# Performance work log

Hardware: AMD Instinct MI355X
Metric: run time of the kernel (lower is better)

The kernel has to match this reference:

```python
import jax, jax.numpy as jnp
import numpy as np

HEADS = 16
DIM_HEAD = 64
SCALE = DIM_HEAD ** -0.5


def setup_inputs() -> dict:
    key = jax.random.key(0)
    ks = jax.random.split(key, 7)
    B, Nq, Dq = 16, 4096, 1024
    Nc, Dc = 77, 768
    inner = HEADS * DIM_HEAD  # 1024
    return {
        "x": jax.random.normal(ks[0], (B, Nq, Dq), jnp.float32),
        "context": jax.random.normal(ks[1], (B, Nc, Dc), jnp.float32),
        "Wq": jax.random.normal(ks[2], (Dq, inner), jnp.float32) * (Dq ** -0.5),
        "Wk": jax.random.normal(ks[3], (Dc, inner), jnp.float32) * (Dc ** -0.5),
        "Wv": jax.random.normal(ks[4], (Dc, inner), jnp.float32) * (Dc ** -0.5),
        "Wo": jax.random.normal(ks[5], (inner, Dq), jnp.float32) * (inner ** -0.5),
        "bo": jnp.zeros((Dq,), jnp.float32),
    }


def reference(x, context, Wq, Wk, Wv, Wo, bo):
    B, Nq, _ = x.shape
    Nc = context.shape[1]
    # projections (no bias), split heads: [B, H, N, Dh]
    q = (x @ Wq).reshape(B, Nq, HEADS, DIM_HEAD).transpose(0, 2, 1, 3)
    k = (context @ Wk).reshape(B, Nc, HEADS, DIM_HEAD).transpose(0, 2, 1, 3)
    v = (context @ Wv).reshape(B, Nc, HEADS, DIM_HEAD).transpose(0, 2, 1, 3)
    sim = jnp.einsum('bhid,bhjd->bhij', q, k) * SCALE
    attn = jax.nn.softmax(sim, axis=-1)
    out = jnp.einsum('bhij,bhjd->bhid', attn, v)
    out = out.transpose(0, 2, 1, 3).reshape(B, Nq, HEADS * DIM_HEAD)
    # to_out linear (dropout is identity at eval)
    return out @ Wo + bo
```

## Files before the change

### kernel.cpp

```cpp
#include <hip/hip_runtime.h>

typedef unsigned short u16;
typedef __bf16 bf16x8 __attribute__((ext_vector_type(8)));
typedef unsigned short u16x8 __attribute__((ext_vector_type(8)));
typedef float f32x4 __attribute__((ext_vector_type(4)));

namespace {
constexpr int kB = 16;
constexpr int kHeads = 16, kDh = 64;
constexpr int kNcPadS = 80;
constexpr int kNcPadV = 96;

constexpr size_t oWqT = 0;
constexpr size_t oWoT = oWqT + (size_t)1024 * 1024 * 2;
constexpr size_t oWkT = oWoT + (size_t)1024 * 1024 * 2;
constexpr size_t oWvT = oWkT + (size_t)1024 * 768 * 2;
constexpr size_t oCtx = oWvT + (size_t)1024 * 768 * 2;
constexpr size_t oKp  = oCtx + (size_t)1232 * 768 * 2;
constexpr size_t oVp  = oKp + (size_t)kB * kHeads * kNcPadS * kDh * 2;
constexpr size_t oQ   = oVp + (size_t)kB * kHeads * kDh * kNcPadV * 2;
}

__device__ __forceinline__ u16 f2b(float f) {
    __bf16 h = (__bf16)f;
    return __builtin_bit_cast(u16, h);
}
__device__ __forceinline__ bf16x8 ldfrag(const u16* p) {
    return __builtin_bit_cast(bf16x8, *reinterpret_cast<const u16x8*>(p));
}
__device__ __forceinline__ f32x4 mfma16(bf16x8 a, bf16x8 b, f32x4 c) {
    return __builtin_amdgcn_mfma_f32_16x16x32_bf16(a, b, c, 0, 0, 0);
}
__device__ __forceinline__ void gload16(const u16* g, u16* lds) {
    __builtin_amdgcn_global_load_lds(
        (const __attribute__((address_space(1))) void*)g,
        (__attribute__((address_space(3))) void*)lds, 16, 0, 0);
}

#define VMCNT(N) asm volatile("s_waitcnt vmcnt(" #N ")" ::: "memory")
#define BARRIER  do { __builtin_amdgcn_s_barrier(); asm volatile("" ::: "memory"); } while (0)

__device__ __forceinline__ void stage_u(const u16* gp, u16* unit, int tid, int kt) {
#pragma unroll
    for (int i = 0; i < 2; ++i) {
        int g = tid + i * 512;
        int prs = g >> 3;
        int s0 = (g & 7) ^ (prs & 7);
        gload16(gp + (size_t)(prs * 2 + (s0 >> 2)) * 1024 + kt + (s0 & 3) * 8,
                unit + ((g >> 6) << 9));
    }
}
__device__ __forceinline__ int pp16(int row16, int k32) {
    return (row16 >> 1) * 64 + (((((row16 & 1) << 2) | (k32 >> 3)) ^ ((row16 >> 1) & 7)) * 8) + (k32 & 7);
}

__global__ __launch_bounds__(256) void xconv_kernel(const float* __restrict__ x, u16* __restrict__ xb) {
    size_t i = (size_t)blockIdx.x * 256 + threadIdx.x;
    const float4* s = reinterpret_cast<const float4*>(x) + 2 * i;
    float4 v0 = s[0], v1 = s[1];
    u16x8 pk = { f2b(v0.x), f2b(v0.y), f2b(v0.z), f2b(v0.w),
                 f2b(v1.x), f2b(v1.y), f2b(v1.z), f2b(v1.w) };
    *reinterpret_cast<u16x8*>(xb + 8 * i) = pk;
}

__global__ __launch_bounds__(256) void prep2_kernel(
    const float* __restrict__ Wq, const float* __restrict__ Wk,
    const float* __restrict__ Wv, const float* __restrict__ Wo,
    const float* __restrict__ ctx, u16* __restrict__ ws) {
    __shared__ u16 tl[64][72];
    int b = blockIdx.x;
    int tid = threadIdx.x;
    if (b < 896) {
        const float* S; u16* D; int t, DC;
        if (b < 256)       { S = Wq; D = ws + oWqT / 2; t = b;       DC = 1024; }
        else if (b < 512)  { S = Wo; D = ws + oWoT / 2; t = b - 256; DC = 1024; }
        else if (b < 704)  { S = Wk; D = ws + oWkT / 2; t = b - 512; DC = 768;  }
        else               { S = Wv; D = ws + oWvT / 2; t = b - 704; DC = 768;  }
        int tk = t >> 4, tn = t & 15;
        int k0 = tk * 64, n0 = tn * 64;
#pragma unroll
        for (int i = 0; i < 4; ++i) {
            int r = (tid >> 4) + i * 16;
            float4 v = *reinterpret_cast<const float4*>(S + (size_t)(k0 + r) * 1024 + n0 + (tid & 15) * 4);
            u16 e0 = f2b(v.x), e1 = f2b(v.y), e2 = f2b(v.z), e3 = f2b(v.w);
            u16* p = &tl[r][(tid & 15) * 4];
            p[0] = e0; p[1] = e1; p[2] = e2; p[3] = e3;
        }
        __syncthreads();
#pragma unroll
        for (int i = 0; i < 2; ++i) {
            int n = (tid >> 3) + i * 32;
            u16x8 o;
#pragma unroll
            for (int j = 0; j < 8; ++j) o[j] = tl[(tid & 7) * 8 + j][n];
            *reinterpret_cast<u16x8*>(D + (size_t)(n0 + n) * DC + k0 + (tid & 7) * 8) = o;
        }
        return;
    }
    if (b < 896 + 462) {
        size_t i = (size_t)(b - 896) * 2048 + tid * 8;
        const float4* s = reinterpret_cast<const float4*>(ctx) + i / 4;
        float4 v0 = s[0], v1 = s[1];
        u16x8 pk = { f2b(v0.x), f2b(v0.y), f2b(v0.z), f2b(v0.w),
                     f2b(v1.x), f2b(v1.y), f2b(v1.z), f2b(v1.w) };
        *reinterpret_cast<u16x8*>(ws + oCtx / 2 + i) = pk;
        return;
    }
    size_t j = (size_t)(b - 896 - 462) * 2048 + tid * 8;
    u16x8 z = {0, 0, 0, 0, 0, 0, 0, 0};
    *reinterpret_cast<u16x8*>(ws + oKp / 2 + j) = z;
}

__global__ __launch_bounds__(64) void kv_kernel(u16* __restrict__ ws) {
    const u16* ctxb = ws + oCtx / 2;
    const u16* WkT = ws + oWkT / 2;
    const u16* WvT = ws + oWvT / 2;
    u16* Kp = ws + oKp / 2;
    u16* Vp = ws + oVp / 2;
    int l = threadIdx.x;
    int mt = blockIdx.x >> 6;
    int nt = blockIdx.x & 63;
    int rowA = mt * 16 + (l & 15);
    int rowB = nt * 16 + (l & 15);
    int koff = (l >> 4) * 8;
    f32x4 accK = {0.f, 0.f, 0.f, 0.f}, accV = {0.f, 0.f, 0.f, 0.f};
    for (int k = 0; k < 768; k += 32) {
        bf16x8 a  = ldfrag(ctxb + rowA * 768 + k + koff);
        bf16x8 bk = ldfrag(WkT + rowB * 768 + k + koff);
        bf16x8 bv = ldfrag(WvT + rowB * 768 + k + koff);
        accK = mfma16(a, bk, accK);
        accV = mfma16(a, bv, accV);
    }
    int c = nt * 16 + (l & 15);
    int h = c >> 6, d = c & 63;
#pragma unroll
    for (int r = 0; r < 4; ++r) {
        int row = mt * 16 + (l >> 4) * 4 + r;
        int b = row / 77, j = row - b * 77;
        Kp[((size_t)(b * 16 + h) * kNcPadS + j) * kDh + d] = f2b(accK[r] * 0.125f);
        Vp[((size_t)(b * 16 + h) * kDh + d) * kNcPadV + j] = f2b(accV[r]);
    }
}

#define GPHASE(RLO, KS, READB, STAGE, VM) do {                                  \
    if (READB) { _Pragma("unroll") for (int c = 0; c < 4; ++c)                  \
        fb[c] = ldfrag(bU##KS + (wn * 4 + c) * 512 + rdoff); }                  \
    _Pragma("unroll") for (int r = 0; r < 4; ++r)                               \
        fa[r] = ldfrag(aU##KS + (wm * 8 + (RLO) + r) * 512 + rdoff);            \
    STAGE;                                                                      \
    BARRIER;                                                                    \
    __builtin_amdgcn_s_setprio(1);                                              \
    _Pragma("unroll") for (int r = 0; r < 4; ++r)                               \
        _Pragma("unroll") for (int c = 0; c < 4; ++c)                           \
            acc[(RLO) + r][c] = mfma16(fa[r], fb[c], acc[(RLO) + r][c]);        \
    __builtin_amdgcn_s_setprio(0);                                              \
    VM;                                                                         \
    BARRIER;                                                                    \
} while (0)

#define GEMM_LOOP(aGp, bGp)                                                                          \
    stage_u(aGp, &sm[0][0][0][0], tid, 0);                                                           \
    stage_u(bGp, &sm[1][0][0][0], tid, 0);                                                           \
    stage_u(aGp, &sm[0][0][1][0], tid, 32);                                                          \
    stage_u(bGp, &sm[1][0][1][0], tid, 32);                                                          \
    stage_u(aGp, &sm[0][1][0][0], tid, 64);                                                          \
    stage_u(bGp, &sm[1][1][0][0], tid, 64);                                                          \
    VMCNT(8); BARRIER;                                                                               \
    for (int t = 0; t < 16; ++t) {                                                                   \
        const int d = t & 1, e = d ^ 1;                                                              \
        const u16* aU0 = &sm[0][d][0][0];                                                            \
        const u16* aU1 = &sm[0][d][1][0];                                                            \
        const u16* bU0 = &sm[1][d][0][0];                                                            \
        const u16* bU1 = &sm[1][d][1][0];                                                            \
        bf16x8 fa[4], fb[4];                                                                         \
        GPHASE(0, 0, true,  { if (t < 15) stage_u(aGp, &sm[0][e][1][0], tid, (t + 1) * 64 + 32); },  \
               {});                                                                                  \
        GPHASE(4, 0, false, { if (t < 15) stage_u(bGp, &sm[1][e][1][0], tid, (t + 1) * 64 + 32); },  \
               { if (t < 15) { VMCNT(8); } else { VMCNT(0); } });                                    \
        GPHASE(0, 1, true,  { if (t < 14) stage_u(aGp, &sm[0][d][0][0], tid, (t + 2) * 64); },       \
               {});                                                                                  \
        GPHASE(4, 1, false, { if (t < 14) stage_u(bGp, &sm[1][d][0][0], tid, (t + 2) * 64); },       \
               { if (t < 14) { VMCNT(8); } else if (t == 14) { VMCNT(4); } });                       \
    }

__global__ __launch_bounds__(512) void qproj_attn_kernel(const u16* __restrict__ xb, u16* __restrict__ ws) {
    __shared__ u16 sm[2][2][2][8192];
    __shared__ u16 Pb[8][1536];
    const u16* WqT = ws + oWqT / 2;
    u16* qb = ws + oQ / 2;
    int tid = threadIdx.x;
    int lane = tid & 63;
    int w = tid >> 6, wm = w >> 2, wn = w & 3;
    int lr = lane & 15, lr2 = lr >> 1;
    const int rdoff = lr2 * 64 + (((((lane & 1) << 2) | (lane >> 4))) ^ lr2) * 8;
    int bid = blockIdx.x;
    int wg = (bid & 7) * 128 + (bid >> 3);
    int bm = wg >> 2, bn = wg & 3;

    const u16* aG = xb + (size_t)(bm * 256) * 1024;
    const u16* bG = WqT + (size_t)(bn * 256) * 1024;

    f32x4 acc[8][4] = {};
    GEMM_LOOP(aG, bG);

    u16* smf = &sm[0][0][0][0];
    u16* qw = smf + (size_t)w * 8192;
    u16* Pw = &Pb[w][0];
    int g = lane >> 4, g8 = g * 8;

#pragma unroll
    for (int r = 0; r < 8; ++r)
#pragma unroll
        for (int c = 0; c < 4; ++c) {
            int d = c * 16 + lr;
            int unit = r * 2 + (d >> 5);
            int k32 = d & 31;
#pragma unroll
            for (int reg = 0; reg < 4; ++reg)
                qw[unit * 512 + pp16(g * 4 + reg, k32)] = f2b(acc[r][c][reg]);
        }
    {
        u16x8 z = {0, 0, 0, 0, 0, 0, 0, 0};
        *reinterpret_cast<u16x8*>(Pw + 2 * 512 + lane * 8) = z;
    }
    int b = bm >> 4;
    int h = bn * 4 + wn;
    const u16* Kh = ws + oKp / 2 + (size_t)(b * 16 + h) * kNcPadS * kDh;
    const u16* Vh = ws + oVp / 2 + (size_t)(b * 16 + h) * kDh * kNcPadV;
    bf16x8 kf[5][2], vf[3][4];
#pragma unroll
    for (int nt = 0; nt < 5; ++nt)
#pragma unroll
        for (int kc = 0; kc < 2; ++kc)
            kf[nt][kc] = ldfrag(Kh + (nt * 16 + lr) * 64 + kc * 32 + g8);
#pragma unroll
    for (int kti = 0; kti < 3; ++kti)
#pragma unroll
        for (int nt = 0; nt < 4; ++nt)
            vf[kti][nt] = ldfrag(Vh + (nt * 16 + lr) * kNcPadV + kti * 32 + g8);
    u16x8 bmask[3];
#pragma unroll
    for (int kti = 0; kti < 3; ++kti)
#pragma unroll
        for (int j = 0; j < 8; ++j)
            bmask[kti][j] = (kti * 32 + g8 + j < 77) ? (u16)0x3F80 : (u16)0;

#pragma unroll 1
    for (int rb = 0; rb < 8; ++rb) {
        f32x4 s[5] = {};
#pragma unroll
        for (int kc = 0; kc < 2; ++kc) {
            bf16x8 a = ldfrag(qw + (rb * 2 + kc) * 512 + rdoff);
#pragma unroll
            for (int nt = 0; nt < 5; ++nt) s[nt] = mfma16(a, kf[nt][kc], s[nt]);
        }
#pragma unroll
        for (int nt = 0; nt < 5; ++nt)
#pragma unroll
            for (int reg = 0; reg < 4; ++reg) {
                int j = nt * 16 + lr;
                Pw[(j >> 5) * 512 + pp16(g * 4 + reg, j & 31)] = f2b(__expf(s[nt][reg]));
            }
        f32x4 o[4] = {};
        f32x4 msum = {0.f, 0.f, 0.f, 0.f};
#pragma unroll
        for (int kti = 0; kti < 3; ++kti) {
            bf16x8 a = ldfrag(Pw + kti * 512 + rdoff);
#pragma unroll
            for (int nt = 0; nt < 4; ++nt) o[nt] = mfma16(a, vf[kti][nt], o[nt]);
            msum = mfma16(a, __builtin_bit_cast(bf16x8, bmask[kti]), msum);
        }
#pragma unroll
        for (int reg = 0; reg < 4; ++reg) {
            float rinv = 1.f / msum[reg];
            int row = bm * 256 + wm * 128 + rb * 16 + g * 4 + reg;
#pragma unroll
            for (int nt = 0; nt < 4; ++nt)
                qb[(size_t)row * 1024 + h * 64 + nt * 16 + lr] = f2b(o[nt][reg] * rinv);
        }
    }
}

__global__ __launch_bounds__(512) void outproj_kernel(u16* __restrict__ ws, const float* __restrict__ bo,
                                                      float* __restrict__ out) {
    __shared__ u16 sm[2][2][2][8192];
    const u16* qb = ws + oQ / 2;
    const u16* WoT = ws + oWoT / 2;
    int tid = threadIdx.x;
    int lane = tid & 63;
    int w = tid >> 6, wm = w >> 2, wn = w & 3;
    int lr = lane & 15, lr2 = lr >> 1;
    const int rdoff = lr2 * 64 + (((((lane & 1) << 2) | (lane >> 4))) ^ lr2) * 8;
    int bid = blockIdx.x;
    int wg = (bid & 7) * 128 + (bid >> 3);
    int bm = wg >> 2, bn = wg & 3;

    const u16* aG = qb + (size_t)(bm * 256) * 1024;
    const u16* bG = WoT + (size_t)(bn * 256) * 1024;

    f32x4 acc[8][4] = {};
    GEMM_LOOP(aG, bG);

#pragma unroll
    for (int c = 0; c < 4; ++c) {
        int col = bn * 256 + wn * 64 + c * 16 + lr;
        float bias = bo[col];
#pragma unroll
        for (int r = 0; r < 8; ++r)
#pragma unroll
            for (int reg = 0; reg < 4; ++reg) {
                int row = bm * 256 + wm * 128 + r * 16 + (lane >> 4) * 4 + reg;
                out[(size_t)row * 1024 + col] = acc[r][c][reg] + bias;
            }
    }
}

extern "C" void kernel_launch(void* const* d_in, const int* in_sizes, int n_in,
                              void* d_out, int out_size, void* d_ws, size_t ws_size,
                              hipStream_t stream) {
    const float* x   = (const float*)d_in[0];
    const float* ctx = (const float*)d_in[1];
    const float* Wq  = (const float*)d_in[2];
    const float* Wk  = (const float*)d_in[3];
    const float* Wv  = (const float*)d_in[4];
    const float* Wo  = (const float*)d_in[5];
    const float* bo  = (const float*)d_in[6];
    float* out = (float*)d_out;
    u16* ws = (u16*)d_ws;
    u16* xb = (u16*)d_out;
    (void)in_sizes; (void)n_in; (void)out_size; (void)ws_size;

    xconv_kernel<<<32768, 256, 0, stream>>>(x, xb);
    prep2_kernel<<<896 + 462 + 1408, 256, 0, stream>>>(Wq, Wk, Wv, Wo, ctx, ws);
    kv_kernel<<<77 * 64, 64, 0, stream>>>(ws);
    qproj_attn_kernel<<<1024, 512, 0, stream>>>(xb, ws);
    outproj_kernel<<<1024, 512, 0, stream>>>(ws, bo, out);
}
```

Before: 502.9 us.

## Fuse fp32-to-bf16 conversion of x into the Q-projection GEMM loader

Drops the separate xconv kernel. The Q-projection GEMM now loads fp32 x straight into registers, packs it to bf16 and writes it into LDS, using a register-staged prefetch two tiles ahead. The goal is to avoid writing and re-reading a 128MB bf16 copy of x plus one kernel launch. In exchange the A operand is read as fp32, doubling its bytes per GEMM, since each x tile is re-read by 4 column blocks. The pipeline also gains extra register pressure and manual waitcnt bookkeeping.

```diff
diff --git a/kernel.cpp b/kernel.cpp
--- a/kernel.cpp
+++ b/kernel.cpp
@@ -36,8 +36,14 @@
         (const __attribute__((address_space(1))) void*)g,
         (__attribute__((address_space(3))) void*)lds, 16, 0, 0);
 }
+__device__ __forceinline__ u16x8 pk8(float4 a, float4 b) {
+    u16x8 p = { f2b(a.x), f2b(a.y), f2b(a.z), f2b(a.w),
+                f2b(b.x), f2b(b.y), f2b(b.z), f2b(b.w) };
+    return p;
+}
 
 #define VMCNT(N) asm volatile("s_waitcnt vmcnt(" #N ")" ::: "memory")
+#define LGKM0    asm volatile("s_waitcnt lgkmcnt(0)" ::: "memory")
 #define BARRIER  do { __builtin_amdgcn_s_barrier(); asm volatile("" ::: "memory"); } while (0)
 
 __device__ __forceinline__ void stage_u(const u16* gp, u16* unit, int tid, int kt) {
@@ -52,15 +58,6 @@
 }
 __device__ __forceinline__ int pp16(int row16, int k32) {
     return (row16 >> 1) * 64 + (((((row16 & 1) << 2) | (k32 >> 3)) ^ ((row16 >> 1) & 7)) * 8) + (k32 & 7);
-}
-
-__global__ __launch_bounds__(256) void xconv_kernel(const float* __restrict__ x, u16* __restrict__ xb) {
-    size_t i = (size_t)blockIdx.x * 256 + threadIdx.x;
-    const float4* s = reinterpret_cast<const float4*>(x) + 2 * i;
-    float4 v0 = s[0], v1 = s[1];
-    u16x8 pk = { f2b(v0.x), f2b(v0.y), f2b(v0.z), f2b(v0.w),
-                 f2b(v1.x), f2b(v1.y), f2b(v1.z), f2b(v1.w) };
-    *reinterpret_cast<u16x8*>(xb + 8 * i) = pk;
 }
 
 __global__ __launch_bounds__(256) void prep2_kernel(
@@ -101,9 +98,7 @@
         size_t i = (size_t)(b - 896) * 2048 + tid * 8;
         const float4* s = reinterpret_cast<const float4*>(ctx) + i / 4;
         float4 v0 = s[0], v1 = s[1];
-        u16x8 pk = { f2b(v0.x), f2b(v0.y), f2b(v0.z), f2b(v0.w),
-                     f2b(v1.x), f2b(v1.y), f2b(v1.z), f2b(v1.w) };
-        *reinterpret_cast<u16x8*>(ws + oCtx / 2 + i) = pk;
+        *reinterpret_cast<u16x8*>(ws + oCtx / 2 + i) = pk8(v0, v1);
         return;
     }
     size_t j = (size_t)(b - 896 - 462) * 2048 + tid * 8;
@@ -183,7 +178,45 @@
                { if (t < 14) { VMCNT(8); } else if (t == 14) { VMCNT(4); } });                       \
     }
 
-__global__ __launch_bounds__(512) void qproj_attn_kernel(const u16* __restrict__ xb, u16* __restrict__ ws) {
+#define QISS(SET, KT) do {                                                                \
+    SET##0 = *reinterpret_cast<const float4*>(aF0 + (KT));                                \
+    SET##1 = *reinterpret_cast<const float4*>(aF0 + (KT) + 4);                            \
+    SET##2 = *reinterpret_cast<const float4*>(aF1 + (KT));                                \
+    SET##3 = *reinterpret_cast<const float4*>(aF1 + (KT) + 4);                            \
+    SET##4 = *reinterpret_cast<const float4*>(aF0 + (KT) + 32);                           \
+    SET##5 = *reinterpret_cast<const float4*>(aF0 + (KT) + 36);                           \
+    SET##6 = *reinterpret_cast<const float4*>(aF1 + (KT) + 32);                           \
+    SET##7 = *reinterpret_cast<const float4*>(aF1 + (KT) + 36);                           \
+} while (0)
+#define QWRT0(SET, BUF) do {                                                              \
+    u16* u_ = &sm[0][BUF][0][0];                                                          \
+    *reinterpret_cast<u16x8*>(u_ + tid * 8) = pk8(SET##0, SET##1);                        \
+    *reinterpret_cast<u16x8*>(u_ + (tid + 512) * 8) = pk8(SET##2, SET##3);                \
+} while (0)
+#define QWRT1(SET, BUF) do {                                                              \
+    u16* u_ = &sm[0][BUF][1][0];                                                          \
+    *reinterpret_cast<u16x8*>(u_ + tid * 8) = pk8(SET##4, SET##5);                        \
+    *reinterpret_cast<u16x8*>(u_ + (tid + 512) * 8) = pk8(SET##6, SET##7);                \
+} while (0)
+
+#define QTILE(T, CUR, NXT) do {                                                           \
+    const int t_ = (T);                                                                   \
+    const int d = t_ & 1, e = d ^ 1;                                                      \
+    const u16* aU0 = &sm[0][d][0][0];                                                     \
+    const u16* aU1 = &sm[0][d][1][0];                                                     \
+    const u16* bU0 = &sm[1][d][0][0];                                                     \
+    const u16* bU1 = &sm[1][d][1][0];                                                     \
+    bf16x8 fa[4], fb[4];                                                                  \
+    GPHASE(0, 0, true,  { if (t_ + 2 <= 15) QISS(NXT, (t_ + 2) * 64); }, {});             \
+    GPHASE(4, 0, false, { if (t_ + 1 <= 15) stage_u(bG, &sm[1][e][1][0], tid, (t_ + 1) * 64 + 32); }, \
+           { if (t_ <= 13) { VMCNT(12); } else if (t_ == 14) { VMCNT(4); } else { VMCNT(0); } });     \
+    GPHASE(0, 1, true,  {}, { if (t_ + 1 <= 15) { QWRT0(CUR, e); LGKM0; } });             \
+    GPHASE(4, 1, false, { if (t_ + 2 <= 15) stage_u(bG, &sm[1][d][0][0], tid, (t_ + 2) * 64); },      \
+           { if (t_ + 1 <= 15) { QWRT1(CUR, e); LGKM0; }                                  \
+             if (t_ <= 13) { VMCNT(12); } else if (t_ == 14) { VMCNT(2); } });            \
+} while (0)
+
+__global__ __launch_bounds__(512) void qproj_attn_kernel(const float* __restrict__ x, u16* __restrict__ ws) {
     __shared__ u16 sm[2][2][2][8192];
     __shared__ u16 Pb[8][1536];
     const u16* WqT = ws + oWqT / 2;
@@ -197,11 +230,31 @@
     int wg = (bid & 7) * 128 + (bid >> 3);
     int bm = wg >> 2, bn = wg & 3;
 
-    const u16* aG = xb + (size_t)(bm * 256) * 1024;
+    int prs = tid >> 3;
+    int s0 = (tid & 7) ^ (prs & 7);
+    const float* aF0 = x + (size_t)(bm * 256 + prs * 2 + (s0 >> 2)) * 1024 + (s0 & 3) * 8;
+    const float* aF1 = aF0 + (size_t)128 * 1024;
     const u16* bG = WqT + (size_t)(bn * 256) * 1024;
 
     f32x4 acc[8][4] = {};
-    GEMM_LOOP(aG, bG);
+    float4 Aq0, Aq1, Aq2, Aq3, Aq4, Aq5, Aq6, Aq7;
+    float4 Bq0, Bq1, Bq2, Bq3, Bq4, Bq5, Bq6, Bq7;
+
+    QISS(Bq, 0);
+    stage_u(bG, &sm[1][0][0][0], tid, 0);
+    stage_u(bG, &sm[1][0][1][0], tid, 32);
+    QISS(Aq, 64);
+    stage_u(bG, &sm[1][1][0][0], tid, 64);
+    VMCNT(14);
+    QWRT0(Bq, 0); QWRT1(Bq, 0);
+    LGKM0;
+    VMCNT(10);
+    BARRIER;
+
+    for (int sp = 0; sp < 8; ++sp) {
+        QTILE(2 * sp, Aq, Bq);
+        QTILE(2 * sp + 1, Bq, Aq);
+    }
 
     u16* smf = &sm[0][0][0][0];
     u16* qw = smf + (size_t)w * 8192;
@@ -212,9 +265,9 @@
     for (int r = 0; r < 8; ++r)
 #pragma unroll
         for (int c = 0; c < 4; ++c) {
-            int d = c * 16 + lr;
-            int unit = r * 2 + (d >> 5);
-            int k32 = d & 31;
+            int dd = c * 16 + lr;
+            int unit = r * 2 + (dd >> 5);
+            int k32 = dd & 31;
 #pragma unroll
             for (int reg = 0; reg < 4; ++reg)
                 qw[unit * 512 + pp16(g * 4 + reg, k32)] = f2b(acc[r][c][reg]);
@@ -327,12 +380,10 @@
     const float* bo  = (const float*)d_in[6];
     float* out = (float*)d_out;
     u16* ws = (u16*)d_ws;
-    u16* xb = (u16*)d_out;
     (void)in_sizes; (void)n_in; (void)out_size; (void)ws_size;
 
-    xconv_kernel<<<32768, 256, 0, stream>>>(x, xb);
     prep2_kernel<<<896 + 462 + 1408, 256, 0, stream>>>(Wq, Wk, Wv, Wo, ctx, ws);
     kv_kernel<<<77 * 64, 64, 0, stream>>>(ws);
-    qproj_attn_kernel<<<1024, 512, 0, stream>>>(xb, ws);
+    qproj_attn_kernel<<<1024, 512, 0, stream>>>(x, ws);
     outproj_kernel<<<1024, 512, 0, stream>>>(ws, bo, out);
 }
```

New measurement: 597.7 us. 1.19x slower.
